# Optimization experiments

Hardware: AMD Instinct MI355X
Metric: run time of the kernel (lower is better)

Reference implementation:

```python
import jax, jax.numpy as jnp
import numpy as np

PATCH = 16
FMAP = 14  # 224 // 16, feature-map / mask resolution
BLUR_K = np.array([[1., 2., 1.], [2., 4., 2.], [1., 2., 1.]], dtype=np.float32) / 16.0  # pascal(3), normalized


def _conv(x, w, stride, pad):
    return jax.lax.conv_general_dilated(
        x, w, (stride, stride), [(pad, pad), (pad, pad)],
        dimension_numbers=("NCHW", "OIHW", "NCHW"))


def _max_blur_pool(x):
    # MaxBlurPool2D(kernel_size=3, stride=2, max_pool_size=2, ceil_mode=False):
    x = jax.lax.reduce_window(x, -jnp.inf, jax.lax.max,
                              (1, 1, 2, 2), (1, 1, 1, 1), "VALID")
    C = x.shape[1]
    kw = jnp.broadcast_to(jnp.asarray(BLUR_K, x.dtype), (C, 1, 3, 3))
    return jax.lax.conv_general_dilated(
        x, kw, (2, 2), [(1, 1), (1, 1)],
        dimension_numbers=("NCHW", "OIHW", "NCHW"), feature_group_count=C)


def _up(m, hw):
    # upsample [B,1,FMAP,FMAP] mask to spatial size hw via repeat_interleave
    f = hw // FMAP
    return jnp.repeat(jnp.repeat(m, f, axis=2), f, axis=3)


def reference(x, masks, w1, w2):
    B = x.shape[0]
    m = masks.reshape(B, 1, FMAP, FMAP).astype(x.dtype)  # fmap-level active mask
    x = x * _up(m, x.shape[2])                 # _apply_masks: zero masked 16x16 patches
    x = _conv(x, w1, 2, 3)                     # B,64,112,112
    x = jax.nn.relu(x * _up(m, x.shape[2]))    # SparK-style sparse conv: re-mask output
    x = _max_blur_pool(x)                      # B,64,56,56
    x = _conv(x, w2, 2, 3)                     # B,768,28,28
    x = jax.nn.relu(x * _up(m, x.shape[2]))    # re-mask output of second sparse conv
    x = _max_blur_pool(x)                      # B,768,14,14
    B_, C, H, W = x.shape
    return x.reshape(B_, C, H * W).transpose(0, 2, 1)  # b (h w) c -> [B,196,768]


def setup_inputs() -> dict:
    key = jax.random.key(0)
    k1, k2, k3, k4 = jax.random.split(key, 4)
    x = jax.random.normal(k1, (64, 3, 224, 224), jnp.float32)
    masks = jax.random.randint(k2, (64, 196), 0, 2).astype(bool)
    # kaiming_normal fan_in scaling as in init_weight
    w1 = jax.random.normal(k3, (64, 3, 7, 7), jnp.float32) * np.float32(np.sqrt(2.0 / (3 * 49)))
    w2 = jax.random.normal(k4, (768, 64, 7, 7), jnp.float32) * np.float32(np.sqrt(2.0 / (64 * 49)))
    return {"x": x, "masks": masks, "w1": w1, "w2": w2}
```

## Files before the change

kernel.cpp:

```cpp
#include <hip/hip_runtime.h>
#include <stdint.h>

typedef __attribute__((ext_vector_type(8))) short short8;
typedef __attribute__((ext_vector_type(4))) float f32x4;

#define DEVFN static __device__ __forceinline__

DEVFN float bf2f(uint16_t u) { union { uint32_t i; float f; } v; v.i = ((uint32_t)u) << 16; return v.f; }
DEVFN uint16_t f2bf(float f) {
  union { float f; uint32_t i; } v; v.f = f;
  uint32_t u = v.i;
  u += 0x7fffu + ((u >> 16) & 1u);
  return (uint16_t)(u >> 16);
}
DEVFN int imin(int a, int b) { return a < b ? a : b; }

DEVFN void gl_lds16(const void* g, void* l) {
  __builtin_amdgcn_global_load_lds(
      (__attribute__((address_space(1))) void*)(void*)g,
      (__attribute__((address_space(3))) void*)l, 16, 0, 0);
}

DEVFN f32x4 mfma16(short8 a, short8 b, f32x4 c) {
  return __builtin_amdgcn_mfma_f32_16x16x32_bf16(a, b, c, 0, 0, 0);
}

static constexpr size_t OFF_XP   = 0;
static constexpr size_t OFF_W1T  = 27557888;
static constexpr size_t OFF_W2T  = 27586560;
static constexpr size_t OFF_Y1   = 32403456;
static constexpr size_t OFF_P1   = 135163904;
static constexpr size_t OFF_Y2   = 166653952;
static constexpr size_t OFF_LIST = 243724288;
static constexpr size_t OFF_CNT  = 243774464;
static constexpr size_t WS_NEED  = 243774468;

__global__ __launch_bounds__(256) void k_list(const int* __restrict__ masks,
                                              int* __restrict__ list, int* __restrict__ count) {
  int gid = blockIdx.x * 256 + threadIdx.x;
  if (masks[gid]) {
    int p = atomicAdd(count, 1);
    list[p] = gid;
  }
}

__global__ __launch_bounds__(256) void k_prep(const float* __restrict__ x, const int* __restrict__ masks,
                                              uint16_t* __restrict__ xp) {
  int gid = blockIdx.x * 256 + threadIdx.x;
  int b = gid / 53824;
  int rc = gid - b * 53824;
  int r2 = rc / 232;
  int c2 = rc - r2 * 232;
  int r = r2 - 3, c = c2 - 3;
  uint16_t o0 = 0, o1 = 0, o2 = 0;
  if ((unsigned)r < 224u && (unsigned)c < 224u) {
    if (masks[b * 196 + (r >> 4) * 14 + (c >> 4)]) {
      const float* px = x + (((size_t)b * 3) * 224 + r) * 224 + c;
      o0 = f2bf(px[0]);
      o1 = f2bf(px[50176]);
      o2 = f2bf(px[100352]);
    }
  }
  ushort4 o; o.x = o0; o.y = o1; o.z = o2; o.w = 0;
  *(ushort4*)(xp + (size_t)gid * 4) = o;
}

__global__ __launch_bounds__(256) void k_wt(const float* __restrict__ w1, const float* __restrict__ w2,
                                            uint16_t* __restrict__ w1t, uint16_t* __restrict__ w2t) {
  int gid = blockIdx.x * 256 + threadIdx.x;
  if (gid < 14336) {
    int kh = gid / 2048; int r = gid - kh * 2048;
    int oc = r >> 5, slot = r & 31;
    int kw = slot >> 2, ic = slot & 3;
    float v = 0.f;
    if (kw < 7 && ic < 3) v = w1[((oc * 3 + ic) * 7 + kh) * 7 + kw];
    w1t[gid] = f2bf(v);
  } else {
    int g2 = gid - 14336;
    int khw = g2 / 49152; int r = g2 - khw * 49152;
    int oc = r >> 6, ic = r & 63;
    int kh = khw / 7, kw = khw - kh * 7;
    w2t[g2] = f2bf(w2[((oc * 64 + ic) * 7 + kh) * 7 + kw]);
  }
}

__global__ __launch_bounds__(256) void k_conv1(const uint16_t* __restrict__ xp, const uint16_t* __restrict__ w1t,
                                               const int* __restrict__ list, const int* __restrict__ count,
                                               uint16_t* __restrict__ y1) {
  __shared__ uint16_t sB[7 * 64 * 32];
  __shared__ uint16_t sA[128 * 32];
  __shared__ int sc[2];

  int cnt = *count;
  int blk = blockIdx.x;
  if (blk * 2 >= cnt) return;
  int tid = threadIdx.x, lane = tid & 63, wave = tid >> 6;
  int csw = (lane & 3) ^ ((lane >> 2) & 3);

  {
    const char* wg = (const char*)w1t;
    char* wl = (char*)sB;
#pragma unroll
    for (int t = 0; t < 7; ++t) {
      int ldsoff = t * 4096 + wave * 1024;
      int goff = t * 4096 + (wave * 16 + (lane >> 2)) * 64 + csw * 16;
      gl_lds16(wg + goff, wl + ldsoff);
    }
  }
  if (tid < 2) sc[tid] = list[imin(blk * 2 + tid, cnt - 1)];
  __syncthreads();

  const char* gA[2];
#pragma unroll
  for (int t = 0; t < 2; ++t) {
    int r = wave * 32 + t * 16 + (lane >> 2);
    int cell = sc[r >> 6];
    int b = cell / 196, cc = cell - b * 196;
    int ci = cc / 14, cj = cc - ci * 14;
    int p = r & 63;
    int oh = ci * 8 + (p >> 3), ow = cj * 8 + (p & 7);
    gA[t] = (const char*)xp + (((size_t)(b * 232 + 2 * oh)) * 232 + 2 * ow) * 8 + csw * 16;
  }

  f32x4 acc[2][4];
#pragma unroll
  for (int i = 0; i < 2; ++i)
#pragma unroll
    for (int j = 0; j < 4; ++j) acc[i][j] = f32x4{0.f, 0.f, 0.f, 0.f};

  int wm = wave * 32;
  int mrow = lane & 15, kg = lane >> 4;
  int sw1 = mrow & 3;

#pragma unroll 1
  for (int kh = 0; kh < 7; ++kh) {
    char* la = (char*)sA + wm * 64;
    gl_lds16(gA[0] + kh * 1856, la);
    gl_lds16(gA[1] + kh * 1856, la + 1024);
    __syncthreads();
    const uint16_t* Bk = sB + kh * 2048;
    int ksw = (kg ^ sw1) * 8;
    short8 a0 = *(const short8*)(sA + (wm + mrow) * 32 + ksw);
    short8 a1 = *(const short8*)(sA + (wm + 16 + mrow) * 32 + ksw);
#pragma unroll
    for (int j = 0; j < 4; ++j) {
      short8 bj = *(const short8*)(Bk + (16 * j + mrow) * 32 + ksw);
      acc[0][j] = mfma16(a0, bj, acc[0][j]);
      acc[1][j] = mfma16(a1, bj, acc[1][j]);
    }
    __syncthreads();
  }

#pragma unroll
  for (int i = 0; i < 2; ++i) {
    int rbase = wm + 16 * i;
    int cellidx = blk * 2 + (rbase >> 6);
    if (cellidx >= cnt) continue;
    int cell = sc[rbase >> 6];
    int b = cell / 196, cc = cell - b * 196;
    int ci = cc / 14, cj = cc - ci * 14;
#pragma unroll
    for (int j = 0; j < 4; ++j) {
      int oc = 16 * j + mrow;
#pragma unroll
      for (int r = 0; r < 4; ++r) {
        int row = rbase + kg * 4 + r;
        int p = row & 63;
        int oh = ci * 8 + (p >> 3), ow = cj * 8 + (p & 7);
        float v = acc[i][j][r];
        v = v > 0.f ? v : 0.f;
        y1[(((size_t)(b * 112 + oh)) * 112 + ow) * 64 + oc] = f2bf(v);
      }
    }
  }
}

__global__ __launch_bounds__(256) void k_pool1(const uint16_t* __restrict__ y1, const int* __restrict__ masks,
                                               uint16_t* __restrict__ p1) {
  __shared__ uint16_t sY[18 * 18 * 64];
  int b = blockIdx.y;
  int tile = blockIdx.x;
  int tr = tile >> 3, tc = tile & 7;
  int pr0 = tr * 8, pc0 = tc * 8;
  int R0 = 2 * pr0 - 7, C0 = 2 * pc0 - 7;
  int tid = threadIdx.x;
  const int* mb = masks + b * 196;

  for (int idx = tid; idx < 2592; idx += 256) {
    int pix = idx >> 3, ch = idx & 7;
    int pr = pix / 18, pc = pix - pr * 18;
    int r = R0 + pr, c = C0 + pc;
    short8 v = {0, 0, 0, 0, 0, 0, 0, 0};
    if ((unsigned)r < 112u && (unsigned)c < 112u && mb[(r >> 3) * 14 + (c >> 3)])
      v = *(const short8*)(y1 + (((size_t)(b * 112 + r)) * 112 + c) * 64 + ch * 8);
    *(short8*)(sY + ((size_t)(pr * 18 + pc)) * 64 + ch * 8) = v;
  }
  __syncthreads();

  for (int it = tid; it < 512; it += 256) {
    int opix = it >> 3, ch = it & 7;
    int lr = opix >> 3, lc = opix & 7;
    int pr = pr0 + lr, pc = pc0 + lc;
    if (pr >= 62 || pc >= 62) continue;
    int oh = pr - 3, ow = pc - 3;
    float acc[8] = {0.f, 0.f, 0.f, 0.f, 0.f, 0.f, 0.f, 0.f};
    if ((unsigned)oh < 56u && (unsigned)ow < 56u) {
      float hm_prev[3][8];
#pragma unroll
      for (int dd = 0; dd < 4; ++dd) {
        float yv[4][8];
        const uint16_t* src = sY + ((size_t)((2 * lr + dd) * 18 + 2 * lc)) * 64 + ch * 8;
#pragma unroll
        for (int e = 0; e < 4; ++e) {
          short8 t8 = *(const short8*)(src + e * 64);
#pragma unroll
          for (int k = 0; k < 8; ++k) yv[e][k] = bf2f((uint16_t)t8[k]);
        }
        float hm[3][8];
#pragma unroll
        for (int e = 0; e < 3; ++e) {
          int qc = 2 * ow - 1 + e;
          float cv = ((unsigned)qc <= 110u) ? 1.f : 0.f;
#pragma unroll
          for (int k = 0; k < 8; ++k) hm[e][k] = cv * fmaxf(yv[e][k], yv[e + 1][k]);
        }
        if (dd > 0) {
          int d = dd - 1;
          int qr = 2 * oh - 1 + d;
          if ((unsigned)qr <= 110u) {
            float wd = (d == 1) ? 2.f : 1.f;
#pragma unroll
            for (int e = 0; e < 3; ++e) {
              float w = wd * ((e == 1) ? 2.f : 1.f);
#pragma unroll
              for (int k = 0; k < 8; ++k) acc[k] += w * fmaxf(hm_prev[e][k], hm[e][k]);
            }
          }
        }
#pragma unroll
        for (int e = 0; e < 3; ++e)
#pragma unroll
          for (int k = 0; k < 8; ++k) hm_prev[e][k] = hm[e][k];
      }
#pragma unroll
      for (int k = 0; k < 8; ++k) acc[k] *= (1.f / 16.f);
    }
    short8 o;
#pragma unroll
    for (int k = 0; k < 8; ++k) o[k] = (short)f2bf(acc[k]);
    *(short8*)(p1 + (((size_t)(b * 62 + pr)) * 62 + pc) * 64 + ch * 8) = o;
  }
}

__global__ __launch_bounds__(256) void k_conv2(const uint16_t* __restrict__ p1, const uint16_t* __restrict__ w2t,
                                               const int* __restrict__ list, const int* __restrict__ count,
                                               uint16_t* __restrict__ y2) {
  __shared__ uint16_t sA[128 * 64];
  __shared__ uint16_t sBt[128 * 64];
  __shared__ int sc[32];

  int cnt = *count;
  int mt = blockIdx.x;
  if (mt * 32 >= cnt) return;
  int tid = threadIdx.x, lane = tid & 63, wave = tid >> 6;
  int ocb = blockIdx.y * 128;
  int csw = (lane & 7) ^ ((lane >> 3) & 7);

  if (tid < 32) sc[tid] = list[imin(mt * 32 + tid, cnt - 1)];
  __syncthreads();

  const char* gA[4]; const char* gB[4];
#pragma unroll
  for (int t = 0; t < 4; ++t) {
    int r = wave * 32 + t * 8 + (lane >> 3);
    int cell = sc[r >> 2];
    int b = cell / 196, cc = cell - b * 196;
    int ci = cc / 14, cj = cc - ci * 14;
    int p = r & 3;
    int oh = 2 * ci + (p >> 1), ow = 2 * cj + (p & 1);
    gA[t] = (const char*)p1 + (((size_t)(b * 62 + 2 * oh)) * 62 + 2 * ow) * 128 + csw * 16;
    int ocr = ocb + wave * 32 + t * 8 + (lane >> 3);
    gB[t] = (const char*)w2t + (size_t)ocr * 128 + csw * 16;
  }

  f32x4 acc[4][4];
#pragma unroll
  for (int i = 0; i < 4; ++i)
#pragma unroll
    for (int j = 0; j < 4; ++j) acc[i][j] = f32x4{0.f, 0.f, 0.f, 0.f};

  int wm = (wave >> 1) * 64, wn = (wave & 1) * 64;
  int mrow = lane & 15, kg = lane >> 4;
  int sw = mrow & 7;
  int kh = 0, kw = 0;

#pragma unroll 1
  for (int it = 0; it < 49; ++it) {
    size_t offA = (size_t)(kh * 62 + kw) * 128;
    size_t offB = (size_t)it * 98304;
    char* la = (char*)sA + (wave * 32) * 128;
    char* lb = (char*)sBt + (wave * 32) * 128;
#pragma unroll
    for (int t = 0; t < 4; ++t) {
      gl_lds16(gA[t] + offA, la + t * 1024);
      gl_lds16(gB[t] + offB, lb + t * 1024);
    }
    __syncthreads();
#pragma unroll
    for (int ks = 0; ks < 2; ++ks) {
      int koff = ((ks * 4 + kg) ^ sw) * 8;
      short8 a[4], bb[4];
#pragma unroll
      for (int i = 0; i < 4; ++i)
        a[i] = *(const short8*)(sA + (wm + 16 * i + mrow) * 64 + koff);
#pragma unroll
      for (int j = 0; j < 4; ++j)
        bb[j] = *(const short8*)(sBt + (wn + 16 * j + mrow) * 64 + koff);
#pragma unroll
      for (int i = 0; i < 4; ++i)
#pragma unroll
        for (int j = 0; j < 4; ++j)
          acc[i][j] = mfma16(a[i], bb[j], acc[i][j]);
    }
    __syncthreads();
    if (++kw == 7) { kw = 0; ++kh; }
  }

#pragma unroll
  for (int i = 0; i < 4; ++i) {
    int rbase = wm + 16 * i;
    int cellslot = (rbase >> 2) + kg;
    int cellidx = mt * 32 + cellslot;
    if (cellidx >= cnt) continue;
    int cell = sc[cellslot];
    int b = cell / 196, cc = cell - b * 196;
    int ci = cc / 14, cj = cc - ci * 14;
#pragma unroll
    for (int j = 0; j < 4; ++j) {
      int oc = ocb + wn + 16 * j + mrow;
#pragma unroll
      for (int r = 0; r < 4; ++r) {
        int oh = 2 * ci + (r >> 1), ow = 2 * cj + (r & 1);
        float v = acc[i][j][r];
        v = v > 0.f ? v : 0.f;
        y2[(((size_t)(b * 784)) + oh * 28 + ow) * 768 + oc] = f2bf(v);
      }
    }
  }
}

__global__ __launch_bounds__(256) void k_pool2(const uint16_t* __restrict__ y2, const int* __restrict__ masks,
                                               float* __restrict__ out) {
  __shared__ uint16_t sY[4 * 28 * 128];
  int chunk = blockIdx.x, pi = blockIdx.y, b = blockIdx.z;
  int ch0 = chunk * 128;
  int tid = threadIdx.x;
  const int* mb = masks + b * 196;

  for (int idx = tid; idx < 1792; idx += 256) {
    int rc = idx >> 4;
    int sub = idx & 15;
    int k = rc / 28, c = rc - k * 28;
    int r = 2 * pi - 1 + k;
    short8 v = {0, 0, 0, 0, 0, 0, 0, 0};
    if ((unsigned)r < 28u && mb[(r >> 1) * 14 + (c >> 1)])
      v = *(const short8*)(y2 + (((size_t)(b * 784)) + r * 28 + c) * 768 + ch0 + sub * 8);
    *(short8*)(sY + ((size_t)(k * 28 + c)) * 128 + sub * 8) = v;
  }
  __syncthreads();

  for (int idx = tid; idx < 1792; idx += 256) {
    int pj = idx >> 7, ch = idx & 127;
    float v[4][4];
#pragma unroll
    for (int e = 0; e < 4; ++e) {
      int col = 2 * pj - 1 + e;
      bool cv = (unsigned)col < 28u;
#pragma unroll
      for (int k = 0; k < 4; ++k)
        v[k][e] = cv ? bf2f(sY[((size_t)(k * 28 + col)) * 128 + ch]) : 0.f;
    }
    float acc = 0.f;
#pragma unroll
    for (int d = 0; d < 3; ++d) {
      int q = 2 * pi - 1 + d;
      float gd = ((unsigned)q <= 26u) ? ((d == 1) ? 2.f : 1.f) : 0.f;
      float s = 0.f;
#pragma unroll
      for (int e = 0; e < 3; ++e) {
        int q2 = 2 * pj - 1 + e;
        float ge = ((unsigned)q2 <= 26u) ? ((e == 1) ? 2.f : 1.f) : 0.f;
        float m = fmaxf(fmaxf(v[d][e], v[d + 1][e]), fmaxf(v[d][e + 1], v[d + 1][e + 1]));
        s += ge * m;
      }
      acc += gd * s;
    }
    out[(((size_t)(b * 196)) + pi * 14 + pj) * 768 + ch0 + ch] = acc * (1.f / 16.f);
  }
}

extern "C" void kernel_launch(void* const* d_in, const int* in_sizes, int n_in,
                              void* d_out, int out_size, void* d_ws, size_t ws_size,
                              hipStream_t stream) {
  const float* x     = (const float*)d_in[0];
  const int*   masks = (const int*)d_in[1];
  const float* w1    = (const float*)d_in[2];
  const float* w2    = (const float*)d_in[3];

  char* ws = (char*)d_ws;
  if (ws_size < WS_NEED) return;

  uint16_t* xp  = (uint16_t*)(ws + OFF_XP);
  uint16_t* w1t = (uint16_t*)(ws + OFF_W1T);
  uint16_t* w2t = (uint16_t*)(ws + OFF_W2T);
  uint16_t* y1  = (uint16_t*)(ws + OFF_Y1);
  uint16_t* p1  = (uint16_t*)(ws + OFF_P1);
  uint16_t* y2  = (uint16_t*)(ws + OFF_Y2);
  int* list     = (int*)(ws + OFF_LIST);
  int* cnt      = (int*)(ws + OFF_CNT);

  hipMemsetAsync(cnt, 0, 4, stream);
  k_list<<<49, 256, 0, stream>>>(masks, list, cnt);
  k_prep<<<13456, 256, 0, stream>>>(x, masks, xp);
  k_wt<<<9464, 256, 0, stream>>>(w1, w2, w1t, w2t);
  k_conv1<<<6272, 256, 0, stream>>>(xp, w1t, list, cnt, y1);
  k_pool1<<<dim3(64, 64), 256, 0, stream>>>(y1, masks, p1);
  k_conv2<<<dim3(392, 6), 256, 0, stream>>>(p1, w2t, list, cnt, y2);
  k_pool2<<<dim3(6, 14, 64), 256, 0, stream>>>(y2, masks, (float*)d_out);
}
```

Measured before the change: 418.9 us.

## Load conv operands directly from global memory and make cell list deterministic

Both convolution kernels drop their LDS staging of the A (and for conv2, B) tiles. They read MFMA operand fragments straight from global memory into registers, which removes the per-iteration barriers and shared-memory traffic. Occupancy hints are added to the launch bounds. The atomic-based active-cell list is replaced with a two-kernel ballot/prefix-sum compaction that produces an ordered list and needs no memset. The cost is more global/L2 load traffic without LDS reuse across waves, and uncoalesced fragment loads.

```diff
diff --git a/kernel.cpp b/kernel.cpp
--- a/kernel.cpp
+++ b/kernel.cpp
@@ -33,15 +33,35 @@
 static constexpr size_t OFF_Y2   = 166653952;
 static constexpr size_t OFF_LIST = 243724288;
 static constexpr size_t OFF_CNT  = 243774464;
-static constexpr size_t WS_NEED  = 243774468;
-
-__global__ __launch_bounds__(256) void k_list(const int* __restrict__ masks,
-                                              int* __restrict__ list, int* __restrict__ count) {
-  int gid = blockIdx.x * 256 + threadIdx.x;
-  if (masks[gid]) {
-    int p = atomicAdd(count, 1);
-    list[p] = gid;
-  }
+static constexpr size_t WS_NEED  = 243774664;
+
+__global__ __launch_bounds__(256) void k_count(const int* __restrict__ masks, int* __restrict__ cnts) {
+  int b = blockIdx.x;
+  int gid = b * 256 + threadIdx.x;
+  unsigned long long m = __ballot(masks[gid] != 0);
+  __shared__ int wsum[4];
+  if ((threadIdx.x & 63) == 0) wsum[threadIdx.x >> 6] = __popcll(m);
+  __syncthreads();
+  if (threadIdx.x == 0) cnts[b] = wsum[0] + wsum[1] + wsum[2] + wsum[3];
+}
+
+__global__ __launch_bounds__(256) void k_emit(const int* __restrict__ masks, const int* __restrict__ cnts,
+                                              int* __restrict__ list, int* __restrict__ total) {
+  int b = blockIdx.x;
+  int gid = b * 256 + threadIdx.x;
+  int lane = threadIdx.x & 63, wave = threadIdx.x >> 6;
+  int base = 0;
+  for (int i = 0; i < b; ++i) base += cnts[i];
+  bool f = masks[gid] != 0;
+  unsigned long long m = __ballot(f);
+  __shared__ int wcnt[4];
+  if (lane == 0) wcnt[wave] = __popcll(m);
+  __syncthreads();
+  int woff = 0;
+  for (int i = 0; i < wave; ++i) woff += wcnt[i];
+  if (f) list[base + woff + __popcll(m & ((1ull << lane) - 1ull))] = gid;
+  if (b == 48 && threadIdx.x == 0)
+    *total = base + wcnt[0] + wcnt[1] + wcnt[2] + wcnt[3];
 }
 
 __global__ __launch_bounds__(256) void k_prep(const float* __restrict__ x, const int* __restrict__ masks,
@@ -84,11 +104,10 @@
   }
 }
 
-__global__ __launch_bounds__(256) void k_conv1(const uint16_t* __restrict__ xp, const uint16_t* __restrict__ w1t,
-                                               const int* __restrict__ list, const int* __restrict__ count,
-                                               uint16_t* __restrict__ y1) {
+__global__ __launch_bounds__(256, 3) void k_conv1(const uint16_t* __restrict__ xp, const uint16_t* __restrict__ w1t,
+                                                  const int* __restrict__ list, const int* __restrict__ count,
+                                                  uint16_t* __restrict__ y1) {
   __shared__ uint16_t sB[7 * 64 * 32];
-  __shared__ uint16_t sA[128 * 32];
   __shared__ int sc[2];
 
   int cnt = *count;
@@ -110,17 +129,20 @@
   if (tid < 2) sc[tid] = list[imin(blk * 2 + tid, cnt - 1)];
   __syncthreads();
 
-  const char* gA[2];
-#pragma unroll
-  for (int t = 0; t < 2; ++t) {
-    int r = wave * 32 + t * 16 + (lane >> 2);
-    int cell = sc[r >> 6];
+  int wm = wave * 32, mrow = lane & 15, kg = lane >> 4;
+
+  const uint16_t* baseA[2];
+#pragma unroll
+  for (int i = 0; i < 2; ++i) {
+    int row = wm + 16 * i + mrow;
+    int cell = sc[row >> 6];
     int b = cell / 196, cc = cell - b * 196;
     int ci = cc / 14, cj = cc - ci * 14;
-    int p = r & 63;
+    int p = row & 63;
     int oh = ci * 8 + (p >> 3), ow = cj * 8 + (p & 7);
-    gA[t] = (const char*)xp + (((size_t)(b * 232 + 2 * oh)) * 232 + 2 * ow) * 8 + csw * 16;
-  }
+    baseA[i] = xp + (((size_t)(b * 232 + 2 * oh)) * 232 + 2 * ow) * 4 + kg * 8;
+  }
+  int ksw = (kg ^ (mrow & 3)) * 8;
 
   f32x4 acc[2][4];
 #pragma unroll
@@ -128,27 +150,17 @@
 #pragma unroll
     for (int j = 0; j < 4; ++j) acc[i][j] = f32x4{0.f, 0.f, 0.f, 0.f};
 
-  int wm = wave * 32;
-  int mrow = lane & 15, kg = lane >> 4;
-  int sw1 = mrow & 3;
-
-#pragma unroll 1
+#pragma unroll
   for (int kh = 0; kh < 7; ++kh) {
-    char* la = (char*)sA + wm * 64;
-    gl_lds16(gA[0] + kh * 1856, la);
-    gl_lds16(gA[1] + kh * 1856, la + 1024);
-    __syncthreads();
+    short8 a0 = *(const short8*)(baseA[0] + kh * 928);
+    short8 a1 = *(const short8*)(baseA[1] + kh * 928);
     const uint16_t* Bk = sB + kh * 2048;
-    int ksw = (kg ^ sw1) * 8;
-    short8 a0 = *(const short8*)(sA + (wm + mrow) * 32 + ksw);
-    short8 a1 = *(const short8*)(sA + (wm + 16 + mrow) * 32 + ksw);
 #pragma unroll
     for (int j = 0; j < 4; ++j) {
       short8 bj = *(const short8*)(Bk + (16 * j + mrow) * 32 + ksw);
       acc[0][j] = mfma16(a0, bj, acc[0][j]);
       acc[1][j] = mfma16(a1, bj, acc[1][j]);
     }
-    __syncthreads();
   }
 
 #pragma unroll
@@ -252,11 +264,9 @@
   }
 }
 
-__global__ __launch_bounds__(256) void k_conv2(const uint16_t* __restrict__ p1, const uint16_t* __restrict__ w2t,
-                                               const int* __restrict__ list, const int* __restrict__ count,
-                                               uint16_t* __restrict__ y2) {
-  __shared__ uint16_t sA[128 * 64];
-  __shared__ uint16_t sBt[128 * 64];
+__global__ __launch_bounds__(256, 2) void k_conv2(const uint16_t* __restrict__ p1, const uint16_t* __restrict__ w2t,
+                                                  const int* __restrict__ list, const int* __restrict__ count,
+                                                  uint16_t* __restrict__ y2) {
   __shared__ int sc[32];
 
   int cnt = *count;
@@ -264,23 +274,26 @@
   if (mt * 32 >= cnt) return;
   int tid = threadIdx.x, lane = tid & 63, wave = tid >> 6;
   int ocb = blockIdx.y * 128;
-  int csw = (lane & 7) ^ ((lane >> 3) & 7);
 
   if (tid < 32) sc[tid] = list[imin(mt * 32 + tid, cnt - 1)];
   __syncthreads();
 
-  const char* gA[4]; const char* gB[4];
-#pragma unroll
-  for (int t = 0; t < 4; ++t) {
-    int r = wave * 32 + t * 8 + (lane >> 3);
-    int cell = sc[r >> 2];
+  int wm = (wave >> 1) * 64, wn = (wave & 1) * 64;
+  int mrow = lane & 15, kg = lane >> 4;
+
+  const uint16_t* baseA[4];
+  const uint16_t* baseB[4];
+#pragma unroll
+  for (int i = 0; i < 4; ++i) {
+    int row = wm + 16 * i + mrow;
+    int cell = sc[row >> 2];
     int b = cell / 196, cc = cell - b * 196;
     int ci = cc / 14, cj = cc - ci * 14;
-    int p = r & 3;
+    int p = row & 3;
     int oh = 2 * ci + (p >> 1), ow = 2 * cj + (p & 1);
-    gA[t] = (const char*)p1 + (((size_t)(b * 62 + 2 * oh)) * 62 + 2 * ow) * 128 + csw * 16;
-    int ocr = ocb + wave * 32 + t * 8 + (lane >> 3);
-    gB[t] = (const char*)w2t + (size_t)ocr * 128 + csw * 16;
+    baseA[i] = p1 + (((size_t)(b * 62 + 2 * oh)) * 62 + 2 * ow) * 64 + kg * 8;
+    int oc = ocb + wn + 16 * i + mrow;
+    baseB[i] = w2t + (size_t)oc * 64 + kg * 8;
   }
 
   f32x4 acc[4][4];
@@ -289,41 +302,28 @@
 #pragma unroll
     for (int j = 0; j < 4; ++j) acc[i][j] = f32x4{0.f, 0.f, 0.f, 0.f};
 
-  int wm = (wave >> 1) * 64, wn = (wave & 1) * 64;
-  int mrow = lane & 15, kg = lane >> 4;
-  int sw = mrow & 7;
-  int kh = 0, kw = 0;
-
 #pragma unroll 1
-  for (int it = 0; it < 49; ++it) {
-    size_t offA = (size_t)(kh * 62 + kw) * 128;
-    size_t offB = (size_t)it * 98304;
-    char* la = (char*)sA + (wave * 32) * 128;
-    char* lb = (char*)sBt + (wave * 32) * 128;
-#pragma unroll
-    for (int t = 0; t < 4; ++t) {
-      gl_lds16(gA[t] + offA, la + t * 1024);
-      gl_lds16(gB[t] + offB, lb + t * 1024);
-    }
-    __syncthreads();
-#pragma unroll
-    for (int ks = 0; ks < 2; ++ks) {
-      int koff = ((ks * 4 + kg) ^ sw) * 8;
-      short8 a[4], bb[4];
-#pragma unroll
-      for (int i = 0; i < 4; ++i)
-        a[i] = *(const short8*)(sA + (wm + 16 * i + mrow) * 64 + koff);
-#pragma unroll
-      for (int j = 0; j < 4; ++j)
-        bb[j] = *(const short8*)(sBt + (wn + 16 * j + mrow) * 64 + koff);
-#pragma unroll
-      for (int i = 0; i < 4; ++i)
+  for (int kh = 0; kh < 7; ++kh) {
+#pragma unroll
+    for (int kw = 0; kw < 7; ++kw) {
+      int offA = (kh * 62 + kw) * 64;
+      int offB = (kh * 7 + kw) * 49152;
+#pragma unroll
+      for (int ks = 0; ks < 2; ++ks) {
+        short8 a[4], bb[4];
+#pragma unroll
+        for (int i = 0; i < 4; ++i)
+          a[i] = *(const short8*)(baseA[i] + offA + ks * 32);
 #pragma unroll
         for (int j = 0; j < 4; ++j)
-          acc[i][j] = mfma16(a[i], bb[j], acc[i][j]);
-    }
-    __syncthreads();
-    if (++kw == 7) { kw = 0; ++kh; }
+          bb[j] = *(const short8*)(baseB[j] + offB + ks * 32);
+#pragma unroll
+        for (int i = 0; i < 4; ++i)
+#pragma unroll
+          for (int j = 0; j < 4; ++j)
+            acc[i][j] = mfma16(a[i], bb[j], acc[i][j]);
+      }
+    }
   }
 
 #pragma unroll
@@ -417,14 +417,15 @@
   uint16_t* p1  = (uint16_t*)(ws + OFF_P1);
   uint16_t* y2  = (uint16_t*)(ws + OFF_Y2);
   int* list     = (int*)(ws + OFF_LIST);
-  int* cnt      = (int*)(ws + OFF_CNT);
-
-  hipMemsetAsync(cnt, 0, 4, stream);
-  k_list<<<49, 256, 0, stream>>>(masks, list, cnt);
+  int* cnts     = (int*)(ws + OFF_CNT);
+  int* total    = cnts + 49;
+
+  k_count<<<49, 256, 0, stream>>>(masks, cnts);
+  k_emit<<<49, 256, 0, stream>>>(masks, cnts, list, total);
   k_prep<<<13456, 256, 0, stream>>>(x, masks, xp);
   k_wt<<<9464, 256, 0, stream>>>(w1, w2, w1t, w2t);
-  k_conv1<<<6272, 256, 0, stream>>>(xp, w1t, list, cnt, y1);
+  k_conv1<<<6272, 256, 0, stream>>>(xp, w1t, list, total, y1);
   k_pool1<<<dim3(64, 64), 256, 0, stream>>>(y1, masks, p1);
-  k_conv2<<<dim3(392, 6), 256, 0, stream>>>(p1, w2t, list, cnt, y2);
+  k_conv2<<<dim3(392, 6), 256, 0, stream>>>(p1, w2t, list, total, y2);
   k_pool2<<<dim3(6, 14, 64), 256, 0, stream>>>(y2, masks, (float*)d_out);
 }
```

Result: slower. 676.8 us (+61.6%).
